# Kernel optimization log

Hardware: AMD Instinct MI355X
Metric: run time of the kernel (lower is better)

Reference implementation:

```python
import jax, jax.numpy as jnp
import numpy as np

T = 4            # number of node types (len(output_sizes))
N = 16384        # nodes per type
D_IN = 512       # input_size
D_H = 1024       # hidden_size
OUT_SIZES = (128, 96, 64, 32)
MAX_OUT = max(OUT_SIZES)


def setup_inputs() -> dict:
    key = jax.random.key(0)
    ks = jax.random.split(key, 16)
    inp = {}
    for t in range(T):
        inp[f"x{t}"] = jax.random.normal(ks[t], (N, D_IN), jnp.float32)
    # nodes are grouped by type (sorted), matching the padded dict layout
    inp["node_type"] = jnp.repeat(jnp.arange(T, dtype=jnp.int64), N)
    # layer1: per-type Linear(input_size, hidden_size) (apply_net)
    inp["W1"] = jax.random.normal(ks[4], (T, D_IN, D_H), jnp.float32) * 0.02
    inp["b1"] = jnp.zeros((T, D_H), jnp.float32)
    # layer2: per-type Linear(hidden_size, out_size_t)
    for t in range(T):
        inp[f"W2_{t}"] = jax.random.normal(ks[5 + t], (D_H, OUT_SIZES[t]), jnp.float32) * 0.02
        inp[f"b2_{t}"] = jnp.zeros((OUT_SIZES[t],), jnp.float32)
    return inp


def reference(x0, x1, x2, x3, node_type, W1, b1,
              W2_0, b2_0, W2_1, b2_1, W2_2, b2_2, W2_3, b2_3):
    # Per-type gather is implicit: x{t} already holds the features of the
    # nodes whose node_type == t (node_type is sorted/blocked).
    xs = jnp.stack([x0, x1, x2, x3])                       # [T, N, D_IN]
    # apply_net: layer1 per type + activation (batched grouped-GEMM)
    h = jax.nn.relu(jnp.einsum('tni,tih->tnh', xs, W1) + b1[:, None, :])  # [T, N, D_H]
    W2s = (W2_0, W2_1, W2_2, W2_3)
    b2s = (b2_0, b2_1, b2_2, b2_3)
    outs = []
    for t in range(T):  # fixed small set of structurally distinct heads
        o = h[t] @ W2s[t] + b2s[t]                         # [N, out_t]
        outs.append(jnp.pad(o, ((0, 0), (0, MAX_OUT - o.shape[1]))))  # _pad to MAX_OUT
    return jnp.stack(outs)                                 # [T, N, MAX_OUT]
```

## Files before the change

### kernel.cpp

```cpp
#include <hip/hip_runtime.h>
#include <hip/hip_bf16.h>


typedef __attribute__((ext_vector_type(8))) short short8;
typedef __attribute__((ext_vector_type(4))) float f32x4;

#define NT 4
#define NNODE 16384
#define DIN 512
#define DH 1024
#define MAXO 128

static __device__ __forceinline__ ushort f2bf(float f) {
    __hip_bfloat16 h = __float2bfloat16(f);
    return *reinterpret_cast<ushort*>(&h);
}

static __device__ __forceinline__ short8 pack8(const float4 a, const float4 b) {
    union { short8 v; ushort u[8]; } r;
    r.u[0] = f2bf(a.x); r.u[1] = f2bf(a.y); r.u[2] = f2bf(a.z); r.u[3] = f2bf(a.w);
    r.u[4] = f2bf(b.x); r.u[5] = f2bf(b.y); r.u[6] = f2bf(b.z); r.u[7] = f2bf(b.w);
    return r.v;
}

#define GLD(gsrc, ldst)                                                        \
    __builtin_amdgcn_global_load_lds(                                          \
        (const __attribute__((address_space(1))) void*)(gsrc),                 \
        (__attribute__((address_space(3))) void*)(ldst), 16, 0, 0)

__global__ __launch_bounds__(256) void cvt_w_t_kernel(
    const float* __restrict__ in, ushort* __restrict__ out,
    int R, int Cin, size_t in_tstride, size_t out_tstride) {
    __shared__ float tile[32][33];
    const int t = blockIdx.z;
    in += (size_t)t * in_tstride;
    out += (size_t)t * out_tstride;
    const int c0 = blockIdx.x * 32, r0 = blockIdx.y * 32;
    const int cx = threadIdx.x & 31;
    const int ry = threadIdx.x >> 5;
#pragma unroll
    for (int j = 0; j < 4; ++j) {
        int rr = ry + j * 8;
        int c = c0 + cx;
        tile[rr][cx] = (c < Cin) ? in[(size_t)(r0 + rr) * Cin + c] : 0.0f;
    }
    __syncthreads();
#pragma unroll
    for (int j = 0; j < 4; ++j) {
        int cc = ry + j * 8;
        out[(size_t)(c0 + cc) * R + r0 + cx] = f2bf(tile[cx][cc]);
    }
}

__global__ __launch_bounds__(256) void cvt_w2_kernel(
    const float* __restrict__ w0, const float* __restrict__ w1,
    const float* __restrict__ w2, const float* __restrict__ w3,
    const float* __restrict__ c0_, const float* __restrict__ c1_,
    const float* __restrict__ c2_, const float* __restrict__ c3_,
    ushort* __restrict__ out, float* __restrict__ b2p) {
    __shared__ float tile[32][33];
    const int t = blockIdx.z;
    const int Cin = (t == 0) ? 128 : (t == 1) ? 96 : (t == 2) ? 64 : 32;
    const float* in = (t == 0) ? w0 : (t == 1) ? w1 : (t == 2) ? w2 : w3;
    ushort* o = out + (size_t)t * MAXO * DH;
    const int c0 = blockIdx.x * 32, r0 = blockIdx.y * 32;
    const int cx = threadIdx.x & 31;
    const int ry = threadIdx.x >> 5;
#pragma unroll
    for (int j = 0; j < 4; ++j) {
        int rr = ry + j * 8;
        int c = c0 + cx;
        tile[rr][cx] = (c < Cin) ? in[(size_t)(r0 + rr) * Cin + c] : 0.0f;
    }
    __syncthreads();
#pragma unroll
    for (int j = 0; j < 4; ++j) {
        int cc = ry + j * 8;
        o[(size_t)(c0 + cc) * DH + r0 + cx] = f2bf(tile[cx][cc]);
    }
    if (blockIdx.x == 0 && blockIdx.y == 0 && threadIdx.x < 128) {
        const float* b = (t == 0) ? c0_ : (t == 1) ? c1_ : (t == 2) ? c2_ : c3_;
        const int n = threadIdx.x;
        b2p[t * 128 + n] = (n < Cin) ? b[n] : 0.0f;
    }
}

__global__ __launch_bounds__(256, 3) void gemm1q(
    const float* __restrict__ x0, const float* __restrict__ x1,
    const float* __restrict__ x2, const float* __restrict__ x3,
    const ushort* __restrict__ W1T, const float* __restrict__ b1,
    ushort* __restrict__ H) {
    constexpr int K = DIN;
    __shared__ char lds[32768];

    const int cpx = gridDim.x >> 3;
    const int g = blockIdx.x;
    const int wg = (g & 7) * cpx + (g >> 3);
    const int t = wg >> 10;
    const int rmn = wg & 1023;
    const int m0 = (rmn >> 3) * 128;
    const int n0 = (rmn & 7) * 128;

    const float* Af = (t == 0) ? x0 : (t == 1) ? x1 : (t == 2) ? x2 : x3;
    const ushort* Bp = W1T + (size_t)t * DH * K;
    const float* bias = b1 + (size_t)t * DH;
    ushort* Ht = H + (size_t)t * NNODE * DH;

    const int tid = threadIdx.x;
    const int lane = tid & 63;
    const int w = tid >> 6;
    const int wm = w >> 1, wn = w & 1;
    const int lrow = lane & 15, lgrp = lane >> 4;

    const float* af32src[4];
    const ushort* bsrc[4];
    int adst[4], bdst[4];
#pragma unroll
    for (int j = 0; j < 4; ++j) {
        const int c = j * 256 + tid;
        const int r = c >> 3;
        const int c8 = c & 7;
        const int cb = (c8 * 16) ^ ((r & 7) << 4);
        af32src[j] = Af + (size_t)(m0 + r) * K + c8 * 8;
        adst[j] = r * 128 + cb;
        bsrc[j] = Bp + (size_t)(n0 + r) * K + (cb >> 1);
        bdst[j] = 16384 + c * 16;
    }

    f32x4 acc[4][4] = {};
    float4 fa[4][2];

#pragma unroll
    for (int j = 0; j < 4; ++j) {
        fa[j][0] = *reinterpret_cast<const float4*>(af32src[j]);
        fa[j][1] = *reinterpret_cast<const float4*>(af32src[j] + 4);
    }

    for (int i = 0; i < K / 64; ++i) {
        const int kt = i * 64;
        const bool more = (i + 1 < K / 64);

#pragma unroll
        for (int j = 0; j < 4; ++j) GLD(bsrc[j] + kt, lds + bdst[j]);
#pragma unroll
        for (int j = 0; j < 4; ++j)
            *reinterpret_cast<short8*>(lds + adst[j]) = pack8(fa[j][0], fa[j][1]);
        asm volatile("" ::: "memory");
        if (more) {
#pragma unroll
            for (int j = 0; j < 4; ++j) {
                fa[j][0] = *reinterpret_cast<const float4*>(af32src[j] + kt + 64);
                fa[j][1] = *reinterpret_cast<const float4*>(af32src[j] + kt + 68);
            }
            asm volatile("s_waitcnt vmcnt(8) lgkmcnt(0)" ::: "memory");
        } else {
            asm volatile("s_waitcnt vmcnt(0) lgkmcnt(0)" ::: "memory");
        }
        __builtin_amdgcn_s_barrier();
        asm volatile("" ::: "memory");

#pragma unroll
        for (int kkk = 0; kkk < 2; ++kkk) {
            short8 bfr[4], af[4];
#pragma unroll
            for (int ni = 0; ni < 4; ++ni) {
                const int br = wn * 64 + ni * 16 + lrow;
                const int kb = (kkk * 64 + lgrp * 16) ^ ((br & 7) << 4);
                bfr[ni] = *(const short8*)(lds + 16384 + br * 128 + kb);
            }
#pragma unroll
            for (int ml = 0; ml < 4; ++ml) {
                const int ar = wm * 64 + ml * 16 + lrow;
                const int kb = (kkk * 64 + lgrp * 16) ^ ((ar & 7) << 4);
                af[ml] = *(const short8*)(lds + ar * 128 + kb);
            }
#pragma unroll
            for (int ml = 0; ml < 4; ++ml)
#pragma unroll
                for (int ni = 0; ni < 4; ++ni)
                    acc[ml][ni] = __builtin_amdgcn_mfma_f32_16x16x32_bf16(
                        bfr[ni], af[ml], acc[ml][ni], 0, 0, 0);
        }

        if (more) {
            asm volatile("" ::: "memory");
            __builtin_amdgcn_s_barrier();
            asm volatile("" ::: "memory");
        }
    }

#pragma unroll
    for (int ni = 0; ni < 4; ++ni) {
        const int ncol = n0 + wn * 64 + ni * 16 + lgrp * 4;
        const float4 bv = *reinterpret_cast<const float4*>(&bias[ncol]);
#pragma unroll
        for (int ml = 0; ml < 4; ++ml) {
            const int row = m0 + wm * 64 + ml * 16 + lrow;
            float v0 = fmaxf(acc[ml][ni][0] + bv.x, 0.0f);
            float v1 = fmaxf(acc[ml][ni][1] + bv.y, 0.0f);
            float v2 = fmaxf(acc[ml][ni][2] + bv.z, 0.0f);
            float v3 = fmaxf(acc[ml][ni][3] + bv.w, 0.0f);
            uint2 p;
            p.x = (uint)f2bf(v0) | ((uint)f2bf(v1) << 16);
            p.y = (uint)f2bf(v2) | ((uint)f2bf(v3) << 16);
            *reinterpret_cast<uint2*>(&Ht[(size_t)row * DH + ncol]) = p;
        }
    }
}

__global__ __launch_bounds__(512, 1) void gemm2k(
    const ushort* __restrict__ Hbase, const ushort* __restrict__ Bbase,
    const float* __restrict__ biasbase, float* __restrict__ Cbase,
    int N, int K, int MT) {
    constexpr int NF = 2;
    constexpr int NBC = 2;
    constexpr int ABYTES = 256 * 64 * 2;
    constexpr int BBYTES = 128 * 64 * 2;
    constexpr int BUF = ABYTES + BBYTES;
    __shared__ char lds[2 * BUF];

    const int cpx = gridDim.x >> 3;
    const int g = blockIdx.x;
    const int wg = (g & 7) * cpx + (g >> 3);
    const int t = wg / MT;
    const int m0 = (wg % MT) * 256;

    const ushort* A = Hbase + (size_t)t * NNODE * DH;
    const ushort* Bp = Bbase + (size_t)t * MAXO * DH;
    const float* bias = biasbase + (size_t)t * MAXO;

    const int tid = threadIdx.x;
    const int lane = tid & 63;
    const int w = tid >> 6;
    const int wm = w >> 2, wn = w & 3;
    const int lrow = lane & 15, lgrp = lane >> 4;

    const ushort* abfsrc[4];
    int adst[4];
#pragma unroll
    for (int j = 0; j < 4; ++j) {
        const int c = j * 512 + tid;
        const int r = c >> 3;
        const int cb = ((c & 7) * 16) ^ ((r & 7) << 4);
        abfsrc[j] = A + (size_t)(m0 + r) * K + (cb >> 1);
        adst[j] = c * 16;
    }
    const ushort* bsrc[NBC];
    int bdst[NBC];
#pragma unroll
    for (int j = 0; j < NBC; ++j) {
        const int c = j * 512 + tid;
        const int r = c >> 3;
        const int cb = ((c & 7) * 16) ^ ((r & 7) << 4);
        bsrc[j] = Bp + (size_t)r * K + (cb >> 1);
        bdst[j] = ABYTES + c * 16;
    }

    f32x4 acc[8][NF] = {};
    const int NK = K / 64;

#pragma unroll
    for (int j = 0; j < 4; ++j) GLD(abfsrc[j], lds + adst[j]);
#pragma unroll
    for (int j = 0; j < NBC; ++j) GLD(bsrc[j], lds + bdst[j]);
    asm volatile("s_waitcnt vmcnt(0)" ::: "memory");
    __builtin_amdgcn_s_barrier();
    asm volatile("" ::: "memory");

    for (int i = 0; i < NK; ++i) {
        const char* cu_ = lds + (i & 1) * BUF;
        char* nx_ = lds + ((i + 1) & 1) * BUF;
        const int ktn = (i + 1) * 64;
        const bool st = (i + 1 < NK);

        if (st) {
#pragma unroll
            for (int j = 0; j < 4; ++j) GLD(abfsrc[j] + ktn, nx_ + adst[j]);
#pragma unroll
            for (int j = 0; j < NBC; ++j) GLD(bsrc[j] + ktn, nx_ + bdst[j]);
        }

#pragma unroll
        for (int kkk = 0; kkk < 2; ++kkk) {
            short8 bfr[NF], af[8];
#pragma unroll
            for (int ni = 0; ni < NF; ++ni) {
                const int br = wn * (NF * 16) + ni * 16 + lrow;
                const int kb = (kkk * 64 + lgrp * 16) ^ ((br & 7) << 4);
                bfr[ni] = *(const short8*)(cu_ + ABYTES + br * 128 + kb);
            }
#pragma unroll
            for (int ml = 0; ml < 8; ++ml) {
                const int ar = wm * 128 + ml * 16 + lrow;
                const int kb = (kkk * 64 + lgrp * 16) ^ ((ar & 7) << 4);
                af[ml] = *(const short8*)(cu_ + ar * 128 + kb);
            }
#pragma unroll
            for (int ml = 0; ml < 8; ++ml)
#pragma unroll
                for (int ni = 0; ni < NF; ++ni)
                    acc[ml][ni] = __builtin_amdgcn_mfma_f32_16x16x32_bf16(
                        bfr[ni], af[ml], acc[ml][ni], 0, 0, 0);
        }

        if (st) {
            asm volatile("s_waitcnt vmcnt(0)" ::: "memory");
            __builtin_amdgcn_s_barrier();
            asm volatile("" ::: "memory");
        }
    }

    const int wnoff = wn * (NF * 16);
    const int wmoff = m0 + wm * 128;
#pragma unroll
    for (int ni = 0; ni < NF; ++ni) {
        const int ncol = wnoff + ni * 16 + lgrp * 4;
        const float4 bv = *reinterpret_cast<const float4*>(&bias[ncol]);
#pragma unroll
        for (int mi = 0; mi < 8; ++mi) {
            const int row = wmoff + mi * 16 + lrow;
            float4 p;
            p.x = acc[mi][ni][0] + bv.x;
            p.y = acc[mi][ni][1] + bv.y;
            p.z = acc[mi][ni][2] + bv.z;
            p.w = acc[mi][ni][3] + bv.w;
            *reinterpret_cast<float4*>(
                &Cbase[(size_t)t * NNODE * MAXO + (size_t)row * N + ncol]) = p;
        }
    }
}

extern "C" void kernel_launch(void* const* d_in, const int* in_sizes, int n_in,
                              void* d_out, int out_size, void* d_ws, size_t ws_size,
                              hipStream_t stream) {
    const float* x0 = (const float*)d_in[0];
    const float* x1 = (const float*)d_in[1];
    const float* x2 = (const float*)d_in[2];
    const float* x3 = (const float*)d_in[3];
    const float* W1 = (const float*)d_in[5];
    const float* b1 = (const float*)d_in[6];
    const float* W2[4] = {(const float*)d_in[7], (const float*)d_in[9],
                          (const float*)d_in[11], (const float*)d_in[13]};
    const float* b2[4] = {(const float*)d_in[8], (const float*)d_in[10],
                          (const float*)d_in[12], (const float*)d_in[14]};

    char* ws = (char*)d_ws;
    ushort* H   = (ushort*)ws;
    ushort* W1T = (ushort*)(ws + 134217728ull);
    ushort* W2T = (ushort*)(ws + 134217728ull + 4194304ull);
    float*  b2p = (float*)(ws + 134217728ull + 4194304ull + 1048576ull);

    cvt_w_t_kernel<<<dim3(32, 16, 4), 256, 0, stream>>>(
        W1, W1T, DIN, DH, (size_t)DIN * DH, (size_t)DH * DIN);
    cvt_w2_kernel<<<dim3(4, 32, 4), 256, 0, stream>>>(
        W2[0], W2[1], W2[2], W2[3], b2[0], b2[1], b2[2], b2[3], W2T, b2p);

    gemm1q<<<4096, 256, 0, stream>>>(x0, x1, x2, x3, W1T, b1, H);

    gemm2k<<<256, 512, 0, stream>>>(H, W2T, b2p, (float*)d_out,
                                    MAXO, DH, NNODE / 256);
}
```

Baseline: 170.4 us.

## Enlarge gemm1 tile to 256x256 with fp32 A staged in LDS via direct loads

```diff
diff --git a/kernel.cpp b/kernel.cpp
--- a/kernel.cpp
+++ b/kernel.cpp
@@ -85,21 +85,21 @@
     }
 }
 
-__global__ __launch_bounds__(256, 3) void gemm1q(
+__global__ __launch_bounds__(512, 1) void gemm1r(
     const float* __restrict__ x0, const float* __restrict__ x1,
     const float* __restrict__ x2, const float* __restrict__ x3,
     const ushort* __restrict__ W1T, const float* __restrict__ b1,
     ushort* __restrict__ H) {
     constexpr int K = DIN;
-    __shared__ char lds[32768];
+    __shared__ char lds[163840];
 
     const int cpx = gridDim.x >> 3;
     const int g = blockIdx.x;
     const int wg = (g & 7) * cpx + (g >> 3);
-    const int t = wg >> 10;
-    const int rmn = wg & 1023;
-    const int m0 = (rmn >> 3) * 128;
-    const int n0 = (rmn & 7) * 128;
+    const int t = wg >> 8;
+    const int rmn = wg & 255;
+    const int m0 = (rmn >> 2) * 256;
+    const int n0 = (rmn & 3) * 256;
 
     const float* Af = (t == 0) ? x0 : (t == 1) ? x1 : (t == 2) ? x2 : x3;
     const ushort* Bp = W1T + (size_t)t * DH * K;
@@ -109,73 +109,72 @@
     const int tid = threadIdx.x;
     const int lane = tid & 63;
     const int w = tid >> 6;
-    const int wm = w >> 1, wn = w & 1;
+    const int wm = w >> 2, wn = w & 3;
     const int lrow = lane & 15, lgrp = lane >> 4;
 
-    const float* af32src[4];
+    const float* asrc[8];
+    int adst[8];
+#pragma unroll
+    for (int j = 0; j < 8; ++j) {
+        const int c = j * 512 + tid;
+        const int r = c >> 4;
+        const int cb = ((c & 15) * 16) ^ ((r & 7) << 4);
+        asrc[j] = Af + (size_t)(m0 + r) * K + (cb >> 2);
+        adst[j] = c * 16;
+    }
     const ushort* bsrc[4];
-    int adst[4], bdst[4];
-#pragma unroll
-    for (int j = 0; j < 4; ++j) {
-        const int c = j * 256 + tid;
+    int bdst[4];
+#pragma unroll
+    for (int j = 0; j < 4; ++j) {
+        const int c = j * 512 + tid;
         const int r = c >> 3;
-        const int c8 = c & 7;
-        const int cb = (c8 * 16) ^ ((r & 7) << 4);
-        af32src[j] = Af + (size_t)(m0 + r) * K + c8 * 8;
-        adst[j] = r * 128 + cb;
+        const int cb = ((c & 7) * 16) ^ ((r & 7) << 4);
         bsrc[j] = Bp + (size_t)(n0 + r) * K + (cb >> 1);
-        bdst[j] = 16384 + c * 16;
-    }
-
-    f32x4 acc[4][4] = {};
-    float4 fa[4][2];
-
-#pragma unroll
-    for (int j = 0; j < 4; ++j) {
-        fa[j][0] = *reinterpret_cast<const float4*>(af32src[j]);
-        fa[j][1] = *reinterpret_cast<const float4*>(af32src[j] + 4);
-    }
-
-    for (int i = 0; i < K / 64; ++i) {
-        const int kt = i * 64;
-        const bool more = (i + 1 < K / 64);
-
-#pragma unroll
-        for (int j = 0; j < 4; ++j) GLD(bsrc[j] + kt, lds + bdst[j]);
-#pragma unroll
-        for (int j = 0; j < 4; ++j)
-            *reinterpret_cast<short8*>(lds + adst[j]) = pack8(fa[j][0], fa[j][1]);
-        asm volatile("" ::: "memory");
+        bdst[j] = 131072 + c * 16;
+    }
+
+    f32x4 acc[8][4] = {};
+    const int NK = K / 64;
+
+#pragma unroll
+    for (int j = 0; j < 8; ++j) GLD(asrc[j], lds + adst[j]);
+#pragma unroll
+    for (int j = 0; j < 4; ++j) GLD(bsrc[j], lds + bdst[j]);
+    asm volatile("s_waitcnt vmcnt(0)" ::: "memory");
+    __builtin_amdgcn_s_barrier();
+    asm volatile("" ::: "memory");
+
+    for (int i = 0; i < NK; ++i) {
+        const char* Al = lds + (i & 1) * 65536;
+        const bool more = (i + 1 < NK);
+
         if (more) {
-#pragma unroll
-            for (int j = 0; j < 4; ++j) {
-                fa[j][0] = *reinterpret_cast<const float4*>(af32src[j] + kt + 64);
-                fa[j][1] = *reinterpret_cast<const float4*>(af32src[j] + kt + 68);
-            }
-            asm volatile("s_waitcnt vmcnt(8) lgkmcnt(0)" ::: "memory");
-        } else {
-            asm volatile("s_waitcnt vmcnt(0) lgkmcnt(0)" ::: "memory");
-        }
-        __builtin_amdgcn_s_barrier();
-        asm volatile("" ::: "memory");
+            const int ofs = (i + 1) * 64;
+            char* An = lds + ((i + 1) & 1) * 65536;
+#pragma unroll
+            for (int j = 0; j < 8; ++j) GLD(asrc[j] + ofs, An + adst[j]);
+        }
 
 #pragma unroll
         for (int kkk = 0; kkk < 2; ++kkk) {
-            short8 bfr[4], af[4];
+            short8 bfr[4], af[8];
 #pragma unroll
             for (int ni = 0; ni < 4; ++ni) {
                 const int br = wn * 64 + ni * 16 + lrow;
                 const int kb = (kkk * 64 + lgrp * 16) ^ ((br & 7) << 4);
-                bfr[ni] = *(const short8*)(lds + 16384 + br * 128 + kb);
+                bfr[ni] = *(const short8*)(lds + 131072 + br * 128 + kb);
             }
 #pragma unroll
-            for (int ml = 0; ml < 4; ++ml) {
-                const int ar = wm * 64 + ml * 16 + lrow;
-                const int kb = (kkk * 64 + lgrp * 16) ^ ((ar & 7) << 4);
-                af[ml] = *(const short8*)(lds + ar * 128 + kb);
+            for (int ml = 0; ml < 8; ++ml) {
+                const int ar = wm * 128 + ml * 16 + lrow;
+                const int base = kkk * 128 + lgrp * 32;
+                const int sw = (ar & 7) << 4;
+                const float4 lo = *(const float4*)(Al + ar * 256 + (base ^ sw));
+                const float4 hi = *(const float4*)(Al + ar * 256 + ((base + 16) ^ sw));
+                af[ml] = pack8(lo, hi);
             }
 #pragma unroll
-            for (int ml = 0; ml < 4; ++ml)
+            for (int ml = 0; ml < 8; ++ml)
 #pragma unroll
                 for (int ni = 0; ni < 4; ++ni)
                     acc[ml][ni] = __builtin_amdgcn_mfma_f32_16x16x32_bf16(
@@ -186,20 +185,28 @@
             asm volatile("" ::: "memory");
             __builtin_amdgcn_s_barrier();
             asm volatile("" ::: "memory");
-        }
-    }
-
+            const int ofs = (i + 1) * 64;
+#pragma unroll
+            for (int j = 0; j < 4; ++j) GLD(bsrc[j] + ofs, lds + bdst[j]);
+            asm volatile("s_waitcnt vmcnt(0)" ::: "memory");
+            __builtin_amdgcn_s_barrier();
+            asm volatile("" ::: "memory");
+        }
+    }
+
+    const int wnoff = n0 + wn * 64;
+    const int wmoff = m0 + wm * 128;
 #pragma unroll
     for (int ni = 0; ni < 4; ++ni) {
-        const int ncol = n0 + wn * 64 + ni * 16 + lgrp * 4;
+        const int ncol = wnoff + ni * 16 + lgrp * 4;
         const float4 bv = *reinterpret_cast<const float4*>(&bias[ncol]);
 #pragma unroll
-        for (int ml = 0; ml < 4; ++ml) {
-            const int row = m0 + wm * 64 + ml * 16 + lrow;
-            float v0 = fmaxf(acc[ml][ni][0] + bv.x, 0.0f);
-            float v1 = fmaxf(acc[ml][ni][1] + bv.y, 0.0f);
-            float v2 = fmaxf(acc[ml][ni][2] + bv.z, 0.0f);
-            float v3 = fmaxf(acc[ml][ni][3] + bv.w, 0.0f);
+        for (int mi = 0; mi < 8; ++mi) {
+            const int row = wmoff + mi * 16 + lrow;
+            float v0 = fmaxf(acc[mi][ni][0] + bv.x, 0.0f);
+            float v1 = fmaxf(acc[mi][ni][1] + bv.y, 0.0f);
+            float v2 = fmaxf(acc[mi][ni][2] + bv.z, 0.0f);
+            float v3 = fmaxf(acc[mi][ni][3] + bv.w, 0.0f);
             uint2 p;
             p.x = (uint)f2bf(v0) | ((uint)f2bf(v1) << 16);
             p.y = (uint)f2bf(v2) | ((uint)f2bf(v3) << 16);
@@ -355,7 +362,7 @@
     cvt_w2_kernel<<<dim3(4, 32, 4), 256, 0, stream>>>(
         W2[0], W2[1], W2[2], W2[3], b2[0], b2[1], b2[2], b2[3], W2T, b2p);
 
-    gemm1q<<<4096, 256, 0, stream>>>(x0, x1, x2, x3, W1T, b1, H);
+    gemm1r<<<1024, 512, 0, stream>>>(x0, x1, x2, x3, W1T, b1, H);
 
     gemm2k<<<256, 512, 0, stream>>>(H, W2T, b2p, (float*)d_out,
                                     MAXO, DH, NNODE / 256);
```

Result: slower. 178.4 us (+4.7%).
